# Kernel optimization log

Hardware: AMD Instinct MI355X
Metric: run time of the kernel (lower is better)

The kernel has to match this reference:

```python
import jax, jax.numpy as jnp
import numpy as np

TILE = 16
NEAR_PLANE = 0.8
FAR_PLANE = 1000.0
ALPHA_THRESHOLD = 1.0 / 255.0
T_THRESHOLD = 1e-4  # transmittance saturation cutoff


def quat_to_rot(q):
    # q = (x, y, z, w)
    x, y, z, w = q[..., 0], q[..., 1], q[..., 2], q[..., 3]
    r0 = jnp.stack([1 - 2 * (y * y + z * z), 2 * (x * y - w * z), 2 * (x * z + w * y)], axis=-1)
    r1 = jnp.stack([2 * (x * y + w * z), 1 - 2 * (x * x + z * z), 2 * (y * z - w * x)], axis=-1)
    r2 = jnp.stack([2 * (x * z - w * y), 2 * (y * z + w * x), 1 - 2 * (x * x + y * y)], axis=-1)
    return jnp.stack([r0, r1, r2], axis=-2)


def sh_basis(d):
    # real SH basis up to degree 3, standard 3DGS ordering/constants
    x, y, z = d[..., 0], d[..., 1], d[..., 2]
    xx, yy, zz = x * x, y * y, z * z
    xy, yz, xz = x * y, y * z, x * z
    return jnp.stack([
        jnp.full_like(x, 0.28209479177387814),
        -0.4886025119029199 * y,
        0.4886025119029199 * z,
        -0.4886025119029199 * x,
        1.0925484305920792 * xy,
        -1.0925484305920792 * yz,
        0.31539156525252005 * (2 * zz - xx - yy),
        -1.0925484305920792 * xz,
        0.5462742152960396 * (xx - yy),
        -0.5900435899266435 * y * (3 * xx - yy),
        2.890611442640554 * xy * z,
        -0.4570457994644658 * y * (4 * zz - xx - yy),
        0.3731763325901154 * z * (2 * zz - 3 * xx - 3 * yy),
        -0.4570457994644658 * x * (4 * zz - xx - yy),
        1.445305721320277 * z * (xx - yy),
        -0.5900435899266435 * x * (xx - 3 * yy),
    ], axis=-1)


def _forward(point_cloud, point_cloud_features, point_invalid_mask,
             camera_intrinsics, q_pointcloud_camera, t_pointcloud_camera,
             camera_height, camera_width, color_max_sh_band):
    N = point_cloud.shape[0]
    # inverse_SE3_qt: camera pose (q,t) gives camera->world; invert to world->camera
    q = q_pointcloud_camera / jnp.linalg.norm(q_pointcloud_camera)
    R_wc = quat_to_rot(q)
    R_cw = R_wc.T
    t_cw = -R_cw @ t_pointcloud_camera
    xyz_cam = point_cloud @ R_cw.T + t_cw  # [N,3]
    zc = xyz_cam[:, 2]
    fx, fy = camera_intrinsics[0, 0], camera_intrinsics[1, 1]
    cx, cy = camera_intrinsics[0, 2], camera_intrinsics[1, 2]
    inv_z = 1.0 / zc
    u = fx * xyz_cam[:, 0] * inv_z + cx
    v = fy * xyz_cam[:, 1] * inv_z + cy
    # filter_point_in_camera: near/far + loose image-bounds culling
    valid = ((point_invalid_mask == 0) & (zc > NEAR_PLANE) & (zc < FAR_PLANE)
             & (u > -4 * TILE) & (u < camera_width + 4 * TILE)
             & (v > -4 * TILE) & (v < camera_height + 4 * TILE))
    # 3D covariance: Sigma = R S S^T R^T with S = diag(exp(log_scale))
    qp = point_cloud_features[:, 0:4]
    qp = qp / jnp.linalg.norm(qp, axis=-1, keepdims=True)
    Rp = quat_to_rot(qp)  # [N,3,3]
    s = jnp.exp(point_cloud_features[:, 4:7])
    M = Rp * s[:, None, :]
    Sigma = jnp.einsum('nij,nkj->nik', M, M)
    Sigma_cam = jnp.einsum('ij,njk,lk->nil', R_cw, Sigma, R_cw)
    # projection Jacobian [N,2,3]
    zero = jnp.zeros_like(zc)
    J = jnp.stack([
        jnp.stack([fx * inv_z, zero, -fx * xyz_cam[:, 0] * inv_z * inv_z], -1),
        jnp.stack([zero, fy * inv_z, -fy * xyz_cam[:, 1] * inv_z * inv_z], -1)], -2)
    cov2d = jnp.einsum('nij,njk,nlk->nil', J, Sigma_cam, J)
    A = cov2d[:, 0, 0] + 0.3  # low-pass filter on 2D cov diagonal
    B = cov2d[:, 0, 1]
    C = cov2d[:, 1, 1] + 0.3
    det = jnp.maximum(A * C - B * B, 1e-9)
    conic_a, conic_b, conic_c = C / det, -B / det, A / det
    mid = 0.5 * (A + C)
    lam_max = mid + jnp.sqrt(jnp.maximum(mid * mid - det, 1e-9))
    radii = jnp.ceil(3.0 * jnp.sqrt(lam_max))
    alpha = jax.nn.sigmoid(point_cloud_features[:, 7])
    # SH color, truncated at color_max_sh_band
    dirs = point_cloud - t_pointcloud_camera
    dirs = dirs / jnp.linalg.norm(dirs, axis=-1, keepdims=True)
    k = (color_max_sh_band + 1) ** 2
    basis = sh_basis(dirs)[:, :k]
    sh = point_cloud_features[:, 8:56].reshape(N, 3, 16)[:, :, :k]
    color = jnp.maximum(jnp.einsum('nk,nck->nc', basis, sh) + 0.5, 0.0)
    # depth sort == per-tile sort-key ordering (key = tile_id | depth)
    order = jnp.argsort(jnp.where(valid, zc, jnp.inf))
    tiles_x = camera_width // TILE
    tiles_y = camera_height // TILE
    t0x = jnp.clip(jnp.floor((u - radii) / TILE), 0, tiles_x - 1)
    t1x = jnp.clip(jnp.floor((u + radii) / TILE), 0, tiles_x - 1)
    t0y = jnp.clip(jnp.floor((v - radii) / TILE), 0, tiles_y - 1)
    t1y = jnp.clip(jnp.floor((v + radii) / TILE), 0, tiles_y - 1)
    xs = tuple(a[order] for a in
               (u, v, conic_a, conic_b, conic_c, alpha, zc,
                valid, t0x, t1x, t0y, t1y)) + (color[order],)
    HW = camera_height * camera_width
    pxf = jnp.tile(jnp.arange(camera_width, dtype=jnp.float32) + 0.5, camera_height)
    pyf = jnp.repeat(jnp.arange(camera_height, dtype=jnp.float32) + 0.5, camera_width)
    txf = jnp.floor(pxf / TILE)
    tyf = jnp.floor(pyf / TILE)

    def body(carry, p):
        T, rgb, dep, acc, cnt = carry
        pu, pv, ca, cb, cc, al, pz, vld, a0x, a1x, a0y, a1y, col = p
        du = pxf - pu
        dv = pyf - pv
        power = -0.5 * (ca * du * du + cc * dv * dv) - cb * du * dv
        ai = jnp.minimum(al * jnp.exp(jnp.minimum(power, 0.0)), 0.99)
        in_tile = (txf >= a0x) & (txf <= a1x) & (tyf >= a0y) & (tyf <= a1y)
        eff = in_tile & (ai >= ALPHA_THRESHOLD) & (T > T_THRESHOLD) & vld
        w = jnp.where(eff, T * ai, 0.0)
        rgb = rgb + w[:, None] * col
        dep = dep + w * pz
        acc = acc + w
        cnt = cnt + eff.astype(jnp.int32)
        T = jnp.where(eff, T * (1.0 - ai), T)
        return (T, rgb, dep, acc, cnt), None

    init = (jnp.ones(HW, dtype=jnp.float32), jnp.zeros((HW, 3), dtype=jnp.float32),
            jnp.zeros(HW, dtype=jnp.float32), jnp.zeros(HW, dtype=jnp.float32),
            jnp.zeros(HW, dtype=jnp.int32))
    (T, rgb, dep, acc, cnt), _ = jax.lax.scan(body, init, xs)
    image = rgb.reshape(camera_height, camera_width, 3)
    depth = (dep / jnp.maximum(acc, 1e-6)).reshape(camera_height, camera_width)
    count = cnt.reshape(camera_height, camera_width)
    return image, depth, count


def setup_inputs() -> dict:
    key = jax.random.key(0)
    k1, k2, k3 = jax.random.split(key, 3)
    N = 2048
    point_cloud = (jax.random.normal(k1, (N, 3), dtype=jnp.float32)
                   * jnp.array([2.0, 2.0, 1.5], dtype=jnp.float32)
                   + jnp.array([0.0, 0.0, 6.0], dtype=jnp.float32))
    feat = jax.random.normal(k2, (N, 56), dtype=jnp.float32) * 0.5
    # log-scales ~ exp(-2) so gaussians cover a few pixels
    feat = feat.at[:, 4:7].set(jax.random.normal(k3, (N, 3), dtype=jnp.float32) * 0.3 - 2.0)
    camera_intrinsics = jnp.array([[200.0, 0.0, 64.0],
                                   [0.0, 200.0, 64.0],
                                   [0.0, 0.0, 1.0]], dtype=jnp.float32)
    return {
        'point_cloud': point_cloud,
        'point_cloud_features': feat,
        'point_object_id': jnp.zeros(N, dtype=jnp.int32),
        'point_invalid_mask': jnp.zeros(N, dtype=jnp.int32),
        'camera_intrinsics': camera_intrinsics,
        'q_pointcloud_camera': jnp.array([0.0, 0.0, 0.0, 1.0], dtype=jnp.float32),
        't_pointcloud_camera': jnp.zeros(3, dtype=jnp.float32),
        'camera_height': 128,
        'camera_width': 128,
        'color_max_sh_band': 2,
    }


def reference(point_cloud, point_cloud_features, point_object_id, point_invalid_mask,
              camera_intrinsics, q_pointcloud_camera, t_pointcloud_camera,
              camera_height, camera_width, color_max_sh_band):
    # point_object_id is used in the original only to pick the per-object pose;
    # with a single camera pose it is inert.
    return _forward(point_cloud, point_cloud_features, point_invalid_mask,
                    camera_intrinsics, q_pointcloud_camera, t_pointcloud_camera,
                    camera_height, camera_width, color_max_sh_band)
```

## Files before the change

### kernel.cpp

```cpp
#include <hip/hip_runtime.h>
#include <math.h>

#define TILE_SZ 16
#define NEARP 0.8f
#define FARP 1000.0f
#define ATHR (1.0f/255.0f)
#define TTHR 0.0001f


#define RANK_CHUNK 2048

__global__ __launch_bounds__(256) void prep_rank_scatter_kernel(
        const float* __restrict__ pc,
        const float* __restrict__ feat,
        const int* __restrict__ invalid_mask,
        const float* __restrict__ K,
        const float* __restrict__ qcam,
        const float* __restrict__ tcam,
        const int* __restrict__ cam_h,
        const int* __restrict__ cam_w,
        const int* __restrict__ sh_band,
        float* __restrict__ sorted_recs,
        int N)
{
    __shared__ float sk[RANK_CHUNK];
    __shared__ int pr[8][33];
    int tid = threadIdx.x;
    int iLocal = tid & 31;
    int slice = tid >> 5;
    int i = blockIdx.x * 32 + iLocal;
    bool live = (i < N);

    if (blockIdx.x == 0 && tid == 0) {
        float4 z = make_float4(0.f, 0.f, 0.f, 0.f);
        float4* s = (float4*)(sorted_recs + (size_t)N * 16);
        s[0] = z; s[1] = z; s[2] = z; s[3] = z;
    }

    float fx = K[0], cx = K[2], fy = K[4], cy = K[5];
    int H = cam_h[0], W = cam_w[0];

    float qx = qcam[0], qy = qcam[1], qz = qcam[2], qw = qcam[3];
    float qn = sqrtf(qx*qx + qy*qy + qz*qz + qw*qw);
    qx /= qn; qy /= qn; qz /= qn; qw /= qn;
    float R00 = 1.f-2.f*(qy*qy+qz*qz), R01 = 2.f*(qx*qy-qw*qz), R02 = 2.f*(qx*qz+qw*qy);
    float R10 = 2.f*(qx*qy+qw*qz), R11 = 1.f-2.f*(qx*qx+qz*qz), R12 = 2.f*(qy*qz-qw*qx);
    float R20 = 2.f*(qx*qz-qw*qy), R21 = 2.f*(qy*qz+qw*qx), R22 = 1.f-2.f*(qx*qx+qy*qy);
    float C00 = R00, C01 = R10, C02 = R20;
    float C10 = R01, C11 = R11, C12 = R21;
    float C20 = R02, C21 = R12, C22 = R22;
    float tx = tcam[0], ty = tcam[1], tz = tcam[2];
    float tcx = -(C00*tx + C01*ty + C02*tz);
    float tcy = -(C10*tx + C11*ty + C12*tz);
    float tcz = -(C20*tx + C21*ty + C22*tz);

    float ki = 0.0f;
    if (live) {
        float px = pc[i*3+0], py = pc[i*3+1], pz = pc[i*3+2];
        float xc = C00*px + C01*py + C02*pz + tcx;
        float yc = C10*px + C11*py + C12*pz + tcy;
        float zc = C20*px + C21*py + C22*pz + tcz;
        float inv_z = 1.0f / zc;
        float u = fx * xc * inv_z + cx;
        float v = fy * yc * inv_z + cy;
        bool valid = (invalid_mask[i] == 0) && (zc > NEARP) && (zc < FARP)
                  && (u > -4.0f*TILE_SZ) && (u < (float)W + 4.0f*TILE_SZ)
                  && (v > -4.0f*TILE_SZ) && (v < (float)H + 4.0f*TILE_SZ);
        ki = valid ? zc : INFINITY;
    }

    int rank_acc = 0;
    for (int cb = 0; cb < N; cb += RANK_CHUNK) {
        int m = min(RANK_CHUNK, N - cb);
        for (int t = tid; t < m; t += 256) {
            int j = cb + t;
            float px = pc[j*3+0], py = pc[j*3+1], pz = pc[j*3+2];
            float xc = C00*px + C01*py + C02*pz + tcx;
            float yc = C10*px + C11*py + C12*pz + tcy;
            float zc = C20*px + C21*py + C22*pz + tcz;
            float inv_z = 1.0f / zc;
            float u = fx * xc * inv_z + cx;
            float v = fy * yc * inv_z + cy;
            bool valid = (invalid_mask[j] == 0) && (zc > NEARP) && (zc < FARP)
                      && (u > -4.0f*TILE_SZ) && (u < (float)W + 4.0f*TILE_SZ)
                      && (v > -4.0f*TILE_SZ) && (v < (float)H + 4.0f*TILE_SZ);
            sk[t] = valid ? zc : INFINITY;
        }
        __syncthreads();
        if (live) {
            int js = slice * (RANK_CHUNK / 8);
            int je = min(js + (RANK_CHUNK / 8), m);
            int j = js;
            for (; j + 4 <= je; j += 4) {
                float4 k4 = *(const float4*)(sk + j);
                int ja = cb + j;
                rank_acc += (k4.x < ki) || (k4.x == ki && (ja    ) < i);
                rank_acc += (k4.y < ki) || (k4.y == ki && (ja + 1) < i);
                rank_acc += (k4.z < ki) || (k4.z == ki && (ja + 2) < i);
                rank_acc += (k4.w < ki) || (k4.w == ki && (ja + 3) < i);
            }
            for (; j < je; j++) {
                float kj = sk[j];
                rank_acc += (kj < ki) || (kj == ki && (cb + j) < i);
            }
        }
        __syncthreads();
    }
    pr[slice][iLocal] = rank_acc;
    __syncthreads();

    if (tid < 32) {
        int ip = blockIdx.x * 32 + tid;
        if (ip < N) {
            int rank = 0;
#pragma unroll
            for (int s = 0; s < 8; s++) rank += pr[s][tid];

            float fv[56];
            const float4* f4 = (const float4*)(feat + (size_t)ip * 56);
#pragma unroll
            for (int k = 0; k < 14; k++) {
                float4 t = f4[k];
                fv[4*k+0] = t.x; fv[4*k+1] = t.y; fv[4*k+2] = t.z; fv[4*k+3] = t.w;
            }
            float px = pc[ip*3+0], py = pc[ip*3+1], pz = pc[ip*3+2];
            float xc = C00*px + C01*py + C02*pz + tcx;
            float yc = C10*px + C11*py + C12*pz + tcy;
            float zc = C20*px + C21*py + C22*pz + tcz;
            float inv_z = 1.0f / zc;
            float u = fx * xc * inv_z + cx;
            float v = fy * yc * inv_z + cy;
            bool valid = (invalid_mask[ip] == 0) && (zc > NEARP) && (zc < FARP)
                      && (u > -4.0f*TILE_SZ) && (u < (float)W + 4.0f*TILE_SZ)
                      && (v > -4.0f*TILE_SZ) && (v < (float)H + 4.0f*TILE_SZ);

            float q0 = fv[0], q1 = fv[1], q2 = fv[2], q3 = fv[3];
            float pn = sqrtf(q0*q0 + q1*q1 + q2*q2 + q3*q3);
            q0 /= pn; q1 /= pn; q2 /= pn; q3 /= pn;
            float P00 = 1.f-2.f*(q1*q1+q2*q2), P01 = 2.f*(q0*q1-q3*q2), P02 = 2.f*(q0*q2+q3*q1);
            float P10 = 2.f*(q0*q1+q3*q2), P11 = 1.f-2.f*(q0*q0+q2*q2), P12 = 2.f*(q1*q2-q3*q0);
            float P20 = 2.f*(q0*q2-q3*q1), P21 = 2.f*(q1*q2+q3*q0), P22 = 1.f-2.f*(q0*q0+q1*q1);
            float s0 = expf(fv[4]), s1 = expf(fv[5]), s2 = expf(fv[6]);
            float M00 = P00*s0, M01 = P01*s1, M02 = P02*s2;
            float M10 = P10*s0, M11 = P11*s1, M12 = P12*s2;
            float M20 = P20*s0, M21 = P21*s1, M22 = P22*s2;
            float S00 = M00*M00 + M01*M01 + M02*M02;
            float S01 = M00*M10 + M01*M11 + M02*M12;
            float S02 = M00*M20 + M01*M21 + M02*M22;
            float S11 = M10*M10 + M11*M11 + M12*M12;
            float S12 = M10*M20 + M11*M21 + M12*M22;
            float S22 = M20*M20 + M21*M21 + M22*M22;
            float T00 = C00*S00 + C01*S01 + C02*S02;
            float T01 = C00*S01 + C01*S11 + C02*S12;
            float T02 = C00*S02 + C01*S12 + C02*S22;
            float T10 = C10*S00 + C11*S01 + C12*S02;
            float T11 = C10*S01 + C11*S11 + C12*S12;
            float T12 = C10*S02 + C11*S12 + C12*S22;
            float T20 = C20*S00 + C21*S01 + C22*S02;
            float T21 = C20*S01 + C21*S11 + C22*S12;
            float T22 = C20*S02 + C21*S12 + C22*S22;
            float G00 = T00*C00 + T01*C01 + T02*C02;
            float G01 = T00*C10 + T01*C11 + T02*C12;
            float G02 = T00*C20 + T01*C21 + T02*C22;
            float G11 = T10*C10 + T11*C11 + T12*C12;
            float G12 = T10*C20 + T11*C21 + T12*C22;
            float G22 = T20*C20 + T21*C21 + T22*C22;
            float j00 = fx * inv_z;
            float j02 = -fx * xc * inv_z * inv_z;
            float j11 = fy * inv_z;
            float j12 = -fy * yc * inv_z * inv_z;
            float a0 = j00*G00 + j02*G02;
            float a1 = j00*G01 + j02*G12;
            float a2 = j00*G02 + j02*G22;
            float b1 = j11*G11 + j12*G12;
            float b2 = j11*G12 + j12*G22;
            float cov00 = a0*j00 + a2*j02;
            float cov01 = a1*j11 + a2*j12;
            float cov11 = b1*j11 + b2*j12;

            float A = cov00 + 0.3f;
            float B = cov01;
            float Cc = cov11 + 0.3f;
            float det = fmaxf(A*Cc - B*B, 1e-9f);
            float conic_a = Cc / det;
            float conic_b = -B / det;
            float conic_c = A / det;
            float mid = 0.5f * (A + Cc);
            float lam = mid + sqrtf(fmaxf(mid*mid - det, 1e-9f));
            float radii = ceilf(3.0f * sqrtf(lam));

            float alpha = 1.0f / (1.0f + expf(-fv[7]));

            float dnx = px - tx, dny = py - ty, dnz = pz - tz;
            float dn = sqrtf(dnx*dnx + dny*dny + dnz*dnz);
            float dx = dnx/dn, dy = dny/dn, dz = dnz/dn;
            float xx = dx*dx, yy = dy*dy, zz = dz*dz;
            float xy = dx*dy, yz = dy*dz, xz = dx*dz;
            float basis[16];
            basis[0] = 0.28209479177387814f;
            basis[1] = -0.4886025119029199f * dy;
            basis[2] = 0.4886025119029199f * dz;
            basis[3] = -0.4886025119029199f * dx;
            basis[4] = 1.0925484305920792f * xy;
            basis[5] = -1.0925484305920792f * yz;
            basis[6] = 0.31539156525252005f * (2.f*zz - xx - yy);
            basis[7] = -1.0925484305920792f * xz;
            basis[8] = 0.5462742152960396f * (xx - yy);
            basis[9] = -0.5900435899266435f * dy * (3.f*xx - yy);
            basis[10] = 2.890611442640554f * xy * dz;
            basis[11] = -0.4570457994644658f * dy * (4.f*zz - xx - yy);
            basis[12] = 0.3731763325901154f * dz * (2.f*zz - 3.f*xx - 3.f*yy);
            basis[13] = -0.4570457994644658f * dx * (4.f*zz - xx - yy);
            basis[14] = 1.445305721320277f * dz * (xx - yy);
            basis[15] = -0.5900435899266435f * dx * (xx - 3.f*yy);
            int band = sh_band[0];
            int kc = (band + 1) * (band + 1);
            float c0 = 0.f, c1 = 0.f, c2 = 0.f;
#pragma unroll
            for (int j = 0; j < 16; j++) {
                if (j < kc) {
                    c0 += basis[j] * fv[8 + 0*16 + j];
                    c1 += basis[j] * fv[8 + 1*16 + j];
                    c2 += basis[j] * fv[8 + 2*16 + j];
                }
            }
            c0 = fmaxf(c0 + 0.5f, 0.0f);
            c1 = fmaxf(c1 + 0.5f, 0.0f);
            c2 = fmaxf(c2 + 0.5f, 0.0f);

            float tiles_x = (float)(W / TILE_SZ);
            float tiles_y = (float)(H / TILE_SZ);
            float t0x = fminf(fmaxf(floorf((u - radii) / TILE_SZ), 0.0f), tiles_x - 1.0f);
            float t1x = fminf(fmaxf(floorf((u + radii) / TILE_SZ), 0.0f), tiles_x - 1.0f);
            float t0y = fminf(fmaxf(floorf((v - radii) / TILE_SZ), 0.0f), tiles_y - 1.0f);
            float t1y = fminf(fmaxf(floorf((v + radii) / TILE_SZ), 0.0f), tiles_y - 1.0f);

            unsigned pb;
            float rmax2;
            if (valid) {
                pb = (unsigned)(int)t0x | ((unsigned)(int)t1x << 8)
                   | ((unsigned)(int)t0y << 16) | ((unsigned)(int)t1y << 24);
                rmax2 = 2.0f * lam * logf(255.0f * alpha);
                if (!(rmax2 >= 0.0f)) rmax2 = -1.0f;
                else rmax2 = rmax2 * 1.0005f + 1e-3f;
            } else {
                pb = 0x00FF00FFu;
                rmax2 = -1.0f;
                alpha = 0.0f;
            }

            float4* dst = (float4*)(sorted_recs + (size_t)rank * 16);
            dst[0] = make_float4(u, v, conic_a, conic_b);
            dst[1] = make_float4(conic_c, alpha, zc, c0);
            dst[2] = make_float4(c1, c2, 0.f, 0.f);
            dst[3] = make_float4(u, v, rmax2, __uint_as_float(pb));
        }
    }
}

#define NSEG 8
#define SEG_CAP 520

#define PH1(P0,P1) do { \
    float du = pxf - P0.x; \
    float dv = pyf - P0.y; \
    float power = -0.5f * (P0.z*du*du + P1.x*dv*dv) - P0.w*du*dv; \
    float e = __expf(power); \
    float ai = fminf(fminf(P1.y * e, P1.y), 0.99f); \
    Tp = (ai >= ATHR) ? Tp * (1.0f - ai) : Tp; \
} while (0)

#define LDG2(D0,D1, WIDX) do { \
    int _ix = ((unsigned)(WIDX) == 0xFFFFu) ? N : (int)(WIDX); \
    const float4* _p = (const float4*)(sorted_recs + (size_t)_ix * 16); \
    D0 = _p[0]; D1 = _p[1]; } while (0)

#define COMPOSITE(P0,P1,P2) do { \
    float du = pxf - P0.x; \
    float dv = pyf - P0.y; \
    float power = -0.5f * (P0.z*du*du + P1.x*dv*dv) - P0.w*du*dv; \
    float e = __expf(power); \
    float ai = fminf(fminf(P1.y * e, P1.y), 0.99f); \
    bool eff = (ai >= ATHR) && (T > TTHR); \
    float w = eff ? T * ai : 0.0f; \
    cr  += w * P1.w; \
    cg  += w * P2.x; \
    cbl += w * P2.y; \
    dep += w * P1.z; \
    acc += w; \
    cnt_px += eff; \
    T = eff ? T * (1.0f - ai) : T; \
} while (0)

__global__ __launch_bounds__(512) void raster_kernel(
        const float* __restrict__ sorted_recs, int N,
        const int* __restrict__ cam_h,
        const int* __restrict__ cam_w,
        float* __restrict__ out)
{
    int W = cam_w[0], H = cam_h[0];
    int tiles_x = W / TILE_SZ;
    int sub = blockIdx.x & 3;
    int tile = blockIdx.x >> 2;
    int bx = tile % tiles_x;
    int by = tile / tiles_x;
    int tid = threadIdx.x;
    int lane = tid & 63;
    int wv = tid >> 6;
    int qpx0 = bx * TILE_SZ + (sub & 1) * 8;
    int qpy0 = by * TILE_SZ + (sub >> 1) * 8;
    int px = qpx0 + (lane & 7);
    int py = qpy0 + (lane >> 3);
    float pxf = (float)px + 0.5f;
    float pyf = (float)py + 0.5f;
    float qx0 = (float)qpx0 + 0.5f, qx1 = (float)qpx0 + 7.5f;
    float qy0 = (float)qpy0 + 0.5f, qy1 = (float)qpy0 + 7.5f;

    __shared__ unsigned short wlist[NSEG][SEG_CAP];
    __shared__ float swave[NSEG][2][64 * 16];
    __shared__ float TP[NSEG][64];
    __shared__ float part[NSEG][6][64];

    unsigned short* wl = wlist[wv];

    int SEGSZ = (N + NSEG - 1) / NSEG;
    int segStart = wv * SEGSZ;
    int segEnd = min(N, segStart + SEGSZ);

    int cnt = 0;
    for (int base = segStart; base < segEnd; base += 256) {
        float4 g[4];
#pragma unroll
        for (int r = 0; r < 4; r++) {
            int idx = base + r * 64 + lane;
            if (idx < segEnd) {
                g[r] = *(const float4*)(sorted_recs + (size_t)idx * 16 + 12);
            } else {
                g[r].x = 0.f; g[r].y = 0.f; g[r].z = -1.f;
                g[r].w = __uint_as_float(0x00FF00FFu);
            }
        }
#pragma unroll
        for (int r = 0; r < 4; r++) {
            unsigned ub = __float_as_uint(g[r].w);
            int b0x = (int)(ub & 0xFFu);
            int b1x = (int)((ub >> 8) & 0xFFu);
            int b0y = (int)((ub >> 16) & 0xFFu);
            int b1y = (int)((ub >> 24) & 0xFFu);
            bool inbox = (bx >= b0x) && (bx <= b1x) && (by >= b0y) && (by <= b1y);
            float dxc = g[r].x - fminf(fmaxf(g[r].x, qx0), qx1);
            float dyc = g[r].y - fminf(fmaxf(g[r].y, qy0), qy1);
            float r2 = dxc*dxc + dyc*dyc;
            bool pred = inbox && (r2 <= g[r].z);
            unsigned long long mm = __ballot(pred);
            if (pred) {
                int below = __popcll(mm & ((1ull << lane) - 1ull));
                wl[cnt + below] = (unsigned short)(base + r * 64 + lane);
            }
            cnt += __popcll(mm);
        }
    }

    float Tp = 1.0f;
    if (wv != NSEG - 1 && cnt > 0) {
        int cntp = (cnt + 7) & ~7;
        if (lane < (cntp - cnt)) wl[cnt + lane] = (unsigned short)0xFFFFu;
        float4 Aa0,Aa1, Ab0,Ab1, Ac0,Ac1, Ad0,Ad1;
        float4 Ba0,Ba1, Bb0,Bb1, Bc0,Bc1, Bd0,Bd1;
        {
            ushort4 ix = *(const ushort4*)(wl);
            LDG2(Aa0,Aa1, ix.x); LDG2(Ab0,Ab1, ix.y);
            LDG2(Ac0,Ac1, ix.z); LDG2(Ad0,Ad1, ix.w);
        }
        bool pdead = false;
        for (int g4 = 0; g4 + 4 < cntp && !pdead; g4 += 8) {
            {
                ushort4 jx = *(const ushort4*)(wl + g4 + 4);
                LDG2(Ba0,Ba1, jx.x); LDG2(Bb0,Bb1, jx.y);
                LDG2(Bc0,Bc1, jx.z); LDG2(Bd0,Bd1, jx.w);
            }
            PH1(Aa0,Aa1); PH1(Ab0,Ab1); PH1(Ac0,Ac1); PH1(Ad0,Ad1);
            if (g4 + 8 < cntp) {
                ushort4 kx = *(const ushort4*)(wl + g4 + 8);
                LDG2(Aa0,Aa1, kx.x); LDG2(Ab0,Ab1, kx.y);
                LDG2(Ac0,Ac1, kx.z); LDG2(Ad0,Ad1, kx.w);
            }
            PH1(Ba0,Ba1); PH1(Bb0,Bb1); PH1(Bc0,Bc1); PH1(Bd0,Bd1);
            pdead = __all(Tp <= TTHR);
        }
    }
    TP[wv][lane] = Tp;
    __syncthreads();

    float T = 1.0f;
    for (int s = 0; s < wv; s++) T *= TP[s][lane];

    float cr = 0.f, cg = 0.f, cbl = 0.f;
    float dep = 0.f, acc = 0.f;
    int cnt_px = 0;

    float* st0 = &swave[wv][0][0];
    float* st1 = &swave[wv][1][0];
    int r0 = lane >> 2;
    int part4 = lane & 3;

    bool wdead = __all(T <= TTHR);
    if (cnt > 0 && !wdead) {
        float4 n0, n1, n2, n3;
        if (r0 < cnt)      n0 = ((const float4*)(sorted_recs + (size_t)wl[r0] * 16))[part4];
        if (16 + r0 < cnt) n1 = ((const float4*)(sorted_recs + (size_t)wl[16 + r0] * 16))[part4];
        if (32 + r0 < cnt) n2 = ((const float4*)(sorted_recs + (size_t)wl[32 + r0] * 16))[part4];
        if (48 + r0 < cnt) n3 = ((const float4*)(sorted_recs + (size_t)wl[48 + r0] * 16))[part4];
        if (r0 < cnt)      *(float4*)(st0 + (lane) * 4)       = n0;
        if (16 + r0 < cnt) *(float4*)(st0 + (64 + lane) * 4)  = n1;
        if (32 + r0 < cnt) *(float4*)(st0 + (128 + lane) * 4) = n2;
        if (48 + r0 < cnt) *(float4*)(st0 + (192 + lane) * 4) = n3;

        int buf = 0;
        for (int c = 0; c < cnt && !wdead; c += 64) {
            int ecnt = min(64, cnt - c);
            float* cur = buf ? st1 : st0;
            float* oth = buf ? st0 : st1;
            int cn = c + 64;
            int rem = cnt - cn;

            float4 m0, m1, m2, m3;
            if (rem > 0) {
                if (r0 < rem)      m0 = ((const float4*)(sorted_recs + (size_t)wl[cn + r0] * 16))[part4];
                if (16 + r0 < rem) m1 = ((const float4*)(sorted_recs + (size_t)wl[cn + 16 + r0] * 16))[part4];
                if (32 + r0 < rem) m2 = ((const float4*)(sorted_recs + (size_t)wl[cn + 32 + r0] * 16))[part4];
                if (48 + r0 < rem) m3 = ((const float4*)(sorted_recs + (size_t)wl[cn + 48 + r0] * 16))[part4];
            }

            for (int j = 0; j < ecnt; j++) {
                const float* p = cur + j * 16;
                float4 p0 = *(const float4*)p;
                float4 p1 = *(const float4*)(p + 4);
                float4 p2 = *(const float4*)(p + 8);
                COMPOSITE(p0, p1, p2);
            }
            wdead = __all(T <= TTHR);

            if (rem > 0) {
                if (r0 < rem)      *(float4*)(oth + (lane) * 4)       = m0;
                if (16 + r0 < rem) *(float4*)(oth + (64 + lane) * 4)  = m1;
                if (32 + r0 < rem) *(float4*)(oth + (128 + lane) * 4) = m2;
                if (48 + r0 < rem) *(float4*)(oth + (192 + lane) * 4) = m3;
            }
            buf ^= 1;
        }
    }

    part[wv][0][lane] = cr;
    part[wv][1][lane] = cg;
    part[wv][2][lane] = cbl;
    part[wv][3][lane] = dep;
    part[wv][4][lane] = acc;
    part[wv][5][lane] = (float)cnt_px;
    __syncthreads();

    if (wv == 0) {
        float o0 = 0.f, o1 = 0.f, o2 = 0.f, o3 = 0.f, o4 = 0.f, o5 = 0.f;
#pragma unroll
        for (int s = 0; s < NSEG; s++) {
            o0 += part[s][0][lane];
            o1 += part[s][1][lane];
            o2 += part[s][2][lane];
            o3 += part[s][3][lane];
            o4 += part[s][4][lane];
            o5 += part[s][5][lane];
        }
        int pix = py * W + px;
        int HW = H * W;
        out[pix*3 + 0] = o0;
        out[pix*3 + 1] = o1;
        out[pix*3 + 2] = o2;
        out[HW*3 + pix] = o3 / fmaxf(o4, 1e-6f);
        out[HW*4 + pix] = o5;
    }
}

extern "C" void kernel_launch(void* const* d_in, const int* in_sizes, int n_in,
                              void* d_out, int out_size, void* d_ws, size_t ws_size,
                              hipStream_t stream) {
    const float* pc    = (const float*)d_in[0];
    const float* feat  = (const float*)d_in[1];
    const int*   inval = (const int*)d_in[3];
    const float* K     = (const float*)d_in[4];
    const float* qc    = (const float*)d_in[5];
    const float* tc    = (const float*)d_in[6];
    const int*   camH  = (const int*)d_in[7];
    const int*   camW  = (const int*)d_in[8];
    const int*   band  = (const int*)d_in[9];
    float* out = (float*)d_out;

    int N = in_sizes[0] / 3;
    int side = (int)(sqrt((double)(out_size / 5)) + 0.5);
    int H = side, W = side;

    float* sorted_recs = (float*)d_ws;

    int pblocks = (N + 31) / 32;
    prep_rank_scatter_kernel<<<pblocks, 256, 0, stream>>>(
        pc, feat, inval, K, qc, tc, camH, camW, band, sorted_recs, N);

    int tiles = (W / TILE_SZ) * (H / TILE_SZ);
    raster_kernel<<<tiles * 4, 512, 0, stream>>>(sorted_recs, N, camH, camW, out);
}
```

Measured before the change: 29.27 us.

## Double depth segments to 16 waves and composite from direct global loads

Doubles the number of depth segments per 8x8 quad from 8 to 16 wavefronts, raising the block size to 1024 threads so each wave culls and composites half as many Gaussians. The LDS double-buffered staging of records for compositing is removed. Instead each lane loads records straight from global memory with register ping-pong prefetch of 4 records at a time, mirroring the transmittance pass. This cuts LDS usage and barriers-free staging but increases redundant global/L2 loads per lane, raises register pressure, and makes the serial transmittance prefix across segments and the final reduction longer.

```diff
diff --git a/kernel.cpp b/kernel.cpp
--- a/kernel.cpp
+++ b/kernel.cpp
@@ -258,7 +258,7 @@
     }
 }
 
-#define NSEG 8
+#define NSEG 16
 #define SEG_CAP 520
 
 #define PH1(P0,P1) do { \
@@ -274,6 +274,11 @@
     int _ix = ((unsigned)(WIDX) == 0xFFFFu) ? N : (int)(WIDX); \
     const float4* _p = (const float4*)(sorted_recs + (size_t)_ix * 16); \
     D0 = _p[0]; D1 = _p[1]; } while (0)
+
+#define LDG3(D0,D1,D2, WIDX) do { \
+    int _ix = ((unsigned)(WIDX) == 0xFFFFu) ? N : (int)(WIDX); \
+    const float4* _p = (const float4*)(sorted_recs + (size_t)_ix * 16); \
+    D0 = _p[0]; D1 = _p[1]; D2 = _p[2]; } while (0)
 
 #define COMPOSITE(P0,P1,P2) do { \
     float du = pxf - P0.x; \
@@ -292,7 +297,7 @@
     T = eff ? T * (1.0f - ai) : T; \
 } while (0)
 
-__global__ __launch_bounds__(512) void raster_kernel(
+__global__ __launch_bounds__(1024) void raster_kernel(
         const float* __restrict__ sorted_recs, int N,
         const int* __restrict__ cam_h,
         const int* __restrict__ cam_w,
@@ -317,7 +322,6 @@
     float qy0 = (float)qpy0 + 0.5f, qy1 = (float)qpy0 + 7.5f;
 
     __shared__ unsigned short wlist[NSEG][SEG_CAP];
-    __shared__ float swave[NSEG][2][64 * 16];
     __shared__ float TP[NSEG][64];
     __shared__ float part[NSEG][6][64];
 
@@ -361,10 +365,11 @@
         }
     }
 
+    int cntp = (cnt + 7) & ~7;
+    if (lane < (cntp - cnt)) wl[cnt + lane] = (unsigned short)0xFFFFu;
+
     float Tp = 1.0f;
-    if (wv != NSEG - 1 && cnt > 0) {
-        int cntp = (cnt + 7) & ~7;
-        if (lane < (cntp - cnt)) wl[cnt + lane] = (unsigned short)0xFFFFu;
+    if (wv != NSEG - 1 && cntp > 0) {
         float4 Aa0,Aa1, Ab0,Ab1, Ac0,Ac1, Ad0,Ad1;
         float4 Ba0,Ba1, Bb0,Bb1, Bc0,Bc1, Bd0,Bd1;
         {
@@ -399,55 +404,31 @@
     float dep = 0.f, acc = 0.f;
     int cnt_px = 0;
 
-    float* st0 = &swave[wv][0][0];
-    float* st1 = &swave[wv][1][0];
-    int r0 = lane >> 2;
-    int part4 = lane & 3;
-
-    bool wdead = __all(T <= TTHR);
-    if (cnt > 0 && !wdead) {
-        float4 n0, n1, n2, n3;
-        if (r0 < cnt)      n0 = ((const float4*)(sorted_recs + (size_t)wl[r0] * 16))[part4];
-        if (16 + r0 < cnt) n1 = ((const float4*)(sorted_recs + (size_t)wl[16 + r0] * 16))[part4];
-        if (32 + r0 < cnt) n2 = ((const float4*)(sorted_recs + (size_t)wl[32 + r0] * 16))[part4];
-        if (48 + r0 < cnt) n3 = ((const float4*)(sorted_recs + (size_t)wl[48 + r0] * 16))[part4];
-        if (r0 < cnt)      *(float4*)(st0 + (lane) * 4)       = n0;
-        if (16 + r0 < cnt) *(float4*)(st0 + (64 + lane) * 4)  = n1;
-        if (32 + r0 < cnt) *(float4*)(st0 + (128 + lane) * 4) = n2;
-        if (48 + r0 < cnt) *(float4*)(st0 + (192 + lane) * 4) = n3;
-
-        int buf = 0;
-        for (int c = 0; c < cnt && !wdead; c += 64) {
-            int ecnt = min(64, cnt - c);
-            float* cur = buf ? st1 : st0;
-            float* oth = buf ? st0 : st1;
-            int cn = c + 64;
-            int rem = cnt - cn;
-
-            float4 m0, m1, m2, m3;
-            if (rem > 0) {
-                if (r0 < rem)      m0 = ((const float4*)(sorted_recs + (size_t)wl[cn + r0] * 16))[part4];
-                if (16 + r0 < rem) m1 = ((const float4*)(sorted_recs + (size_t)wl[cn + 16 + r0] * 16))[part4];
-                if (32 + r0 < rem) m2 = ((const float4*)(sorted_recs + (size_t)wl[cn + 32 + r0] * 16))[part4];
-                if (48 + r0 < rem) m3 = ((const float4*)(sorted_recs + (size_t)wl[cn + 48 + r0] * 16))[part4];
-            }
-
-            for (int j = 0; j < ecnt; j++) {
-                const float* p = cur + j * 16;
-                float4 p0 = *(const float4*)p;
-                float4 p1 = *(const float4*)(p + 4);
-                float4 p2 = *(const float4*)(p + 8);
-                COMPOSITE(p0, p1, p2);
-            }
+    if (cntp > 0 && !__all(T <= TTHR)) {
+        float4 Aa0,Aa1,Aa2, Ab0,Ab1,Ab2, Ac0,Ac1,Ac2, Ad0,Ad1,Ad2;
+        float4 Ba0,Ba1,Ba2, Bb0,Bb1,Bb2, Bc0,Bc1,Bc2, Bd0,Bd1,Bd2;
+        {
+            ushort4 ix = *(const ushort4*)(wl);
+            LDG3(Aa0,Aa1,Aa2, ix.x); LDG3(Ab0,Ab1,Ab2, ix.y);
+            LDG3(Ac0,Ac1,Ac2, ix.z); LDG3(Ad0,Ad1,Ad2, ix.w);
+        }
+        bool wdead = false;
+        for (int g4 = 0; g4 + 4 < cntp && !wdead; g4 += 8) {
+            {
+                ushort4 jx = *(const ushort4*)(wl + g4 + 4);
+                LDG3(Ba0,Ba1,Ba2, jx.x); LDG3(Bb0,Bb1,Bb2, jx.y);
+                LDG3(Bc0,Bc1,Bc2, jx.z); LDG3(Bd0,Bd1,Bd2, jx.w);
+            }
+            COMPOSITE(Aa0,Aa1,Aa2); COMPOSITE(Ab0,Ab1,Ab2);
+            COMPOSITE(Ac0,Ac1,Ac2); COMPOSITE(Ad0,Ad1,Ad2);
+            if (g4 + 8 < cntp) {
+                ushort4 kx = *(const ushort4*)(wl + g4 + 8);
+                LDG3(Aa0,Aa1,Aa2, kx.x); LDG3(Ab0,Ab1,Ab2, kx.y);
+                LDG3(Ac0,Ac1,Ac2, kx.z); LDG3(Ad0,Ad1,Ad2, kx.w);
+            }
+            COMPOSITE(Ba0,Ba1,Ba2); COMPOSITE(Bb0,Bb1,Bb2);
+            COMPOSITE(Bc0,Bc1,Bc2); COMPOSITE(Bd0,Bd1,Bd2);
             wdead = __all(T <= TTHR);
-
-            if (rem > 0) {
-                if (r0 < rem)      *(float4*)(oth + (lane) * 4)       = m0;
-                if (16 + r0 < rem) *(float4*)(oth + (64 + lane) * 4)  = m1;
-                if (32 + r0 < rem) *(float4*)(oth + (128 + lane) * 4) = m2;
-                if (48 + r0 < rem) *(float4*)(oth + (192 + lane) * 4) = m3;
-            }
-            buf ^= 1;
         }
     }
 
@@ -505,5 +486,5 @@
         pc, feat, inval, K, qc, tc, camH, camW, band, sorted_recs, N);
 
     int tiles = (W / TILE_SZ) * (H / TILE_SZ);
-    raster_kernel<<<tiles * 4, 512, 0, stream>>>(sorted_recs, N, camH, camW, out);
+    raster_kernel<<<tiles * 4, 1024, 0, stream>>>(sorted_recs, N, camH, camW, out);
 }
```

After: 36.98 us. 26.3% more time.
